# Kernel optimization log

Hardware: AMD Instinct MI355X
Metric: run time of the kernel (lower is better)

## Reference

```python
import math
import jax, jax.numpy as jnp
import numpy as np

NUM_BUCKETS = 32
MAX_DISTANCE = 128


def _relative_position_bucket(relative_position):
    # bidirectional=False: positive relative positions map to bucket 0
    rp = -jnp.minimum(relative_position, 0)  # non-negative distances
    max_exact = NUM_BUCKETS // 2
    is_small = rp < max_exact
    # clamp to >=1 before log to avoid log(0); those lanes are selected away by is_small
    rp_large = max_exact + (
        jnp.log(jnp.maximum(rp, 1).astype(jnp.float32) / max_exact)
        / math.log(MAX_DISTANCE / max_exact)
        * (NUM_BUCKETS - max_exact)
    ).astype(jnp.int32)
    rp_large = jnp.minimum(rp_large, NUM_BUCKETS - 1)
    return jnp.where(is_small, rp, rp_large)


def setup_inputs() -> dict:
    key = jax.random.key(0)
    k1, k2, k3, k4 = jax.random.split(key, 4)
    B, L, H, E = 4, 2048, 8, 64
    return {
        "queries": jax.random.normal(k1, (B, L, H, E), dtype=jnp.float32),
        "keys": jax.random.normal(k2, (B, L, H, E), dtype=jnp.float32),
        "values": jax.random.normal(k3, (B, L, H, E), dtype=jnp.float32),
        "bias_table": jax.random.normal(k4, (NUM_BUCKETS, 8), dtype=jnp.float32),
    }


def reference(queries, keys, values, bias_table):
    B, L, H, E = queries.shape
    scale = 1.0 / math.sqrt(E)

    # scores: [B, H, L, S]
    scores = jnp.einsum("blhe,bshe->bhls", queries, keys)

    # causal mask (TriangularCausalMask): masked positions -> -inf BEFORE scaling
    causal = jnp.triu(jnp.ones((L, L), dtype=bool), k=1)  # [L, L]
    scores = jnp.where(causal[None, None], -jnp.inf, scores)

    attn = scale * scores

    # T5-style relative position bias: [1, H, L, L]
    pos = jnp.arange(L)
    rel_pos = pos[None, :] - pos[:, None]  # memory - query
    buckets = _relative_position_bucket(rel_pos)  # [L, L] in [0, 32)
    bias = bias_table[buckets]  # [L, L, 8]
    bias = jnp.transpose(bias, (2, 0, 1))[None]  # [1, 8, L, L]
    attn = attn + bias

    series = jax.nn.softmax(attn, axis=-1)  # dropout p=0.0 -> identity
    V = jnp.einsum("bhls,bshd->blhd", series, values)
    return V
```

## Files before the change

kernel.cpp:

```cpp
#include <hip/hip_runtime.h>
#include <hip/hip_bf16.h>
#include <math.h>

typedef __attribute__((ext_vector_type(8)))  short short8;
typedef __attribute__((ext_vector_type(4)))  float floatx4;
typedef __attribute__((ext_vector_type(16))) float f32x16;

#define L_SEQ 2048
#define NHEADS 8
#define EDIM 64
#define PLANE (L_SEQ * EDIM)
#define LOG2E 1.4426950408889634f

union U8 { unsigned u[4]; short8 s; };

__device__ __forceinline__ unsigned cvt_pk(float lo, float hi) {
    unsigned r;
    asm("v_cvt_pk_bf16_f32 %0, %1, %2" : "=v"(r) : "v"(lo), "v"(hi));
    return r;
}
__device__ __forceinline__ short8 pack8(floatx4 a, floatx4 b) {
    U8 r;
    r.u[0] = cvt_pk(a[0], a[1]); r.u[1] = cvt_pk(a[2], a[3]);
    r.u[2] = cvt_pk(b[0], b[1]); r.u[3] = cvt_pk(b[2], b[3]);
    return r.s;
}
__device__ __forceinline__ float fast_exp2(float x) {
    float r;
    asm("v_exp_f32 %0, %1" : "=v"(r) : "v"(x));
    return r;
}

__global__ __launch_bounds__(256) void prep_frag(
    const float* __restrict__ K, const float* __restrict__ V,
    const float* __restrict__ table,
    unsigned short* __restrict__ Kf, unsigned short* __restrict__ Vf,
    float* __restrict__ Btab)
{
    __shared__ unsigned short Tk[64][72];
    __shared__ unsigned short Tv[64][72];
    const int st  = blockIdx.x;
    const int bh  = blockIdx.y;
    const int b   = bh >> 3, h = bh & 7;
    const int tid = threadIdx.x;
    const int sb  = st * 64;

    if (st == 0 && bh < 8) {
        for (int d = tid; d < L_SEQ; d += 256) {
            int bucket;
            if (d < 16) bucket = d;
            else {
                float t = logf((float)d * 0.0625f) / 2.0794415416798357f * 16.0f;
                int bb = 16 + (int)t;
                bucket = bb < 31 ? bb : 31;
            }
            Btab[bh * L_SEQ + d] = table[bucket * NHEADS + bh] * LOG2E;
        }
    }

    {
        int s0 = tid >> 3, e0 = (tid & 7) * 8;
        #pragma unroll
        for (int j = 0; j < 2; ++j) {
            int s = s0 + j * 32;
            const float* kp = K + ((size_t)(b * L_SEQ + sb + s) * NHEADS + h) * EDIM + e0;
            floatx4 f0 = *(const floatx4*)kp;
            floatx4 f1 = *(const floatx4*)(kp + 4);
            *(short8*)&Tk[s][e0] = pack8(f0, f1);
        }
    }
    {
        int e = tid & 63, sg = tid >> 6;
        #pragma unroll
        for (int j = 0; j < 16; ++j) {
            int s = sg * 16 + j;
            float v = V[((size_t)(b * L_SEQ + sb + s) * NHEADS + h) * EDIM + e];
            union { float f; unsigned u; } cv; cv.f = v;
            Tv[e][s] = (unsigned short)((cv.u + 0x7FFFu + ((cv.u >> 16) & 1u)) >> 16);
        }
    }
    __syncthreads();
    {
        int s2 = tid >> 7, t7 = tid & 127, ec = t7 >> 5, l31 = t7 & 31;
        #pragma unroll
        for (int hi = 0; hi < 2; ++hi) {
            int row = s2 * 32 + l31, e = ec * 16 + hi * 8;
            short8 v = *(const short8*)&Tk[row][e];
            size_t unit = (((size_t)bh * 64 + st * 2 + s2) * 4 + ec) * 64 + hi * 32 + l31;
            *(short8*)&Kf[unit * 8] = v;
        }
    }
    {
        int s2 = tid >> 7, t7 = tid & 127, et = t7 >> 6, lane = t7 & 63;
        #pragma unroll
        for (int c = 0; c < 2; ++c) {
            int e = et * 32 + (lane & 31), k0 = s2 * 32 + c * 16 + (lane >> 5) * 8;
            short8 v = *(const short8*)&Tv[e][k0];
            size_t unit = ((((size_t)bh * 64 + st * 2 + s2) * 2 + et) * 2 + c) * 64 + lane;
            *(short8*)&Vf[unit * 8] = v;
        }
    }
}

__global__ __launch_bounds__(256, 3) void attn_fwd(
    const float* __restrict__ Q, const unsigned short* __restrict__ Kf,
    const unsigned short* __restrict__ Vf, const float* __restrict__ Btab,
    float* __restrict__ Out)
{
    __shared__ __align__(16) float bias_lds[L_SEQ];
    __shared__ __align__(16) float osc[2][32][64];
    __shared__ float lsc[2][2][16];

    const int bid  = blockIdx.x;
    const int wid  = (bid & 7) * 128 + (bid >> 3);
    const int bh   = wid >> 5;
    const int pair = wid & 31;
    const int qgA  = pair, qgB = 63 - pair;
    const int b    = bh >> 3, h = bh & 7;
    const int tid  = threadIdx.x;
    const int w    = tid >> 6, lane = tid & 63;
    const int q32  = lane & 31;
    const int hi   = lane >> 5;
    const int hi4  = 4 * hi, hi8 = 8 * hi;

    const int dmax4 = (32 * (qgB + 1)) >> 2;
    const floatx4* bt = (const floatx4*)(Btab + h * L_SEQ);
    for (int i = tid; i < dmax4; i += 256)
        ((floatx4*)bias_lds)[i] = bt[i];
    __syncthreads();

    const float cbias = bias_lds[1024];

    const unsigned short* kfb = Kf + (size_t)bh * PLANE + lane * 8;
    const unsigned short* vfb = Vf + (size_t)bh * PLANE + lane * 8;

    U8 onesf;
    onesf.u[0] = 0x3F803F80u; onesf.u[1] = 0x3F803F80u;
    onesf.u[2] = 0x3F803F80u; onesf.u[3] = 0x3F803F80u;

    const float qscale = 0.125f * LOG2E;

    #pragma unroll 1
    for (int pass = 0; pass < 2; ++pass) {
        const int qg   = pass ? qgB : qgA;
        const int qs   = qg * 32;
        const int qrow = qs + q32;
        const int nsub = qg + 1;

        const float* qptr = Q + ((size_t)(b * L_SEQ + qrow) * NHEADS + h) * EDIM;
        short8 qfrag[4];
        #pragma unroll
        for (int ec = 0; ec < 4; ++ec) {
            floatx4 f0 = *(const floatx4*)(qptr + ec * 16 + hi8);
            floatx4 f1 = *(const floatx4*)(qptr + ec * 16 + hi8 + 4);
            qfrag[ec] = pack8(f0, f1);
        }

        const int len = (nsub + 3) >> 2;
        const int r0  = w * len;
        const int r1  = (r0 + len < nsub) ? r0 + len : nsub;

        f32x16 o_acc[2] = {};
        f32x16 o_l = {};

        for (int s32 = r0; s32 < r1; ++s32) {
            const int kv0s = s32 * 32;
            const bool far = (s32 <= qg - 5);

            const unsigned short* kp = kfb + (size_t)s32 * 2048;
            const unsigned short* vp = vfb + (size_t)s32 * 2048;
            short8 kf0 = *(const short8*)(kp);
            short8 kf1 = *(const short8*)(kp + 512);
            short8 kf2 = *(const short8*)(kp + 1024);
            short8 kf3 = *(const short8*)(kp + 1536);
            short8 vf0 = *(const short8*)(vp);
            short8 vf1 = *(const short8*)(vp + 512);
            short8 vf2 = *(const short8*)(vp + 1024);
            short8 vf3 = *(const short8*)(vp + 1536);

            f32x16 st = {};
            st = __builtin_amdgcn_mfma_f32_32x32x16_bf16(kf0, qfrag[0], st, 0, 0, 0);
            st = __builtin_amdgcn_mfma_f32_32x32x16_bf16(kf1, qfrag[1], st, 0, 0, 0);
            st = __builtin_amdgcn_mfma_f32_32x32x16_bf16(kf2, qfrag[2], st, 0, 0, 0);
            st = __builtin_amdgcn_mfma_f32_32x32x16_bf16(kf3, qfrag[3], st, 0, 0, 0);

            float p[16];
            if (far) {
                #pragma unroll
                for (int r = 0; r < 16; ++r)
                    p[r] = fast_exp2(fmaf(qscale, st[r], cbias));
            } else if (s32 != qg) {
                const float* bptr = &bias_lds[qrow - kv0s - hi4];
                #pragma unroll
                for (int r = 0; r < 16; ++r)
                    p[r] = fast_exp2(fmaf(qscale, st[r], bptr[-(r & 3) - 8 * (r >> 2)]));
            } else {
                #pragma unroll
                for (int r = 0; r < 16; ++r) {
                    int kidx = (r & 3) + 8 * (r >> 2) + hi4;
                    int d = q32 - kidx;
                    int dc = d < 0 ? 0 : d;
                    float ex = fast_exp2(fmaf(qscale, st[r], bias_lds[dc]));
                    p[r] = (d >= 0) ? ex : 0.0f;
                }
            }

            unsigned x0 = cvt_pk(p[0],  p[1]),  x1 = cvt_pk(p[2],  p[3]);
            unsigned y0 = cvt_pk(p[4],  p[5]),  y1 = cvt_pk(p[6],  p[7]);
            unsigned x2 = cvt_pk(p[8],  p[9]),  x3 = cvt_pk(p[10], p[11]);
            unsigned y2 = cvt_pk(p[12], p[13]), y3 = cvt_pk(p[14], p[15]);
            asm("v_permlane32_swap_b32 %0, %1" : "+v"(x0), "+v"(y0));
            asm("v_permlane32_swap_b32 %0, %1" : "+v"(x1), "+v"(y1));
            asm("v_permlane32_swap_b32 %0, %1" : "+v"(x2), "+v"(y2));
            asm("v_permlane32_swap_b32 %0, %1" : "+v"(x3), "+v"(y3));
            U8 pf0;
            pf0.u[0] = x0; pf0.u[1] = x1; pf0.u[2] = y0; pf0.u[3] = y1;
            U8 pf1;
            pf1.u[0] = x2; pf1.u[1] = x3; pf1.u[2] = y2; pf1.u[3] = y3;

            o_acc[0] = __builtin_amdgcn_mfma_f32_32x32x16_bf16(pf0.s, vf0, o_acc[0], 0, 0, 0);
            o_acc[0] = __builtin_amdgcn_mfma_f32_32x32x16_bf16(pf1.s, vf1, o_acc[0], 0, 0, 0);
            o_acc[1] = __builtin_amdgcn_mfma_f32_32x32x16_bf16(pf0.s, vf2, o_acc[1], 0, 0, 0);
            o_acc[1] = __builtin_amdgcn_mfma_f32_32x32x16_bf16(pf1.s, vf3, o_acc[1], 0, 0, 0);
            o_l      = __builtin_amdgcn_mfma_f32_32x32x16_bf16(pf0.s, onesf.s, o_l, 0, 0, 0);
            o_l      = __builtin_amdgcn_mfma_f32_32x32x16_bf16(pf1.s, onesf.s, o_l, 0, 0, 0);
        }

        __syncthreads();
        if (w & 1) {
            int slot = w >> 1;
            #pragma unroll
            for (int et = 0; et < 2; ++et)
                #pragma unroll
                for (int r = 0; r < 16; ++r)
                    osc[slot][et * 16 + r][lane] = o_acc[et][r];
            if (q32 == 0) {
                #pragma unroll
                for (int r = 0; r < 16; ++r) lsc[slot][hi][r] = o_l[r];
            }
        }
        __syncthreads();
        if (!(w & 1)) {
            int slot = w >> 1;
            #pragma unroll
            for (int et = 0; et < 2; ++et)
                #pragma unroll
                for (int r = 0; r < 16; ++r)
                    o_acc[et][r] += osc[slot][et * 16 + r][lane];
            #pragma unroll
            for (int r = 0; r < 16; ++r) o_l[r] += lsc[slot][hi][r];
        }
        __syncthreads();
        if (w == 2) {
            #pragma unroll
            for (int et = 0; et < 2; ++et)
                #pragma unroll
                for (int r = 0; r < 16; ++r)
                    osc[0][et * 16 + r][lane] = o_acc[et][r];
            if (q32 == 0) {
                #pragma unroll
                for (int r = 0; r < 16; ++r) lsc[0][hi][r] = o_l[r];
            }
        }
        __syncthreads();
        if (w == 0) {
            #pragma unroll
            for (int et = 0; et < 2; ++et)
                #pragma unroll
                for (int r = 0; r < 16; ++r)
                    o_acc[et][r] += osc[0][et * 16 + r][lane];
            #pragma unroll
            for (int r = 0; r < 16; ++r) o_l[r] += lsc[0][hi][r];

            #pragma unroll
            for (int r = 0; r < 16; ++r) {
                int qv = (r & 3) + 8 * (r >> 2) + hi4;
                float iv = 1.0f / o_l[r];
                float* op = Out + ((size_t)(b * L_SEQ + qs + qv) * NHEADS + h) * EDIM + q32;
                op[0]  = o_acc[0][r] * iv;
                op[32] = o_acc[1][r] * iv;
            }
        }
    }
}

extern "C" void kernel_launch(void* const* d_in, const int* in_sizes, int n_in,
                              void* d_out, int out_size, void* d_ws, size_t ws_size,
                              hipStream_t stream) {
    const float* Q     = (const float*)d_in[0];
    const float* K     = (const float*)d_in[1];
    const float* V     = (const float*)d_in[2];
    const float* table = (const float*)d_in[3];
    float* Out = (float*)d_out;
    unsigned short* Kf = (unsigned short*)d_ws;
    unsigned short* Vf = Kf + (size_t)4 * NHEADS * PLANE;
    float* Btab = (float*)(Vf + (size_t)4 * NHEADS * PLANE);
    (void)in_sizes; (void)n_in; (void)out_size; (void)ws_size;

    dim3 pgrid(32, 32);
    prep_frag<<<pgrid, 256, 0, stream>>>(K, V, table, Kf, Vf, Btab);
    attn_fwd<<<dim3(1024), 256, 0, stream>>>(Q, Kf, Vf, Btab, Out);
}
```

Measured before the change: 57.82 us.

## Process two adjacent query tiles per pass to reuse K/V fragment loads

```diff
diff --git a/kernel.cpp b/kernel.cpp
--- a/kernel.cpp
+++ b/kernel.cpp
@@ -102,7 +102,7 @@
     }
 }
 
-__global__ __launch_bounds__(256, 3) void attn_fwd(
+__global__ __launch_bounds__(256, 2) void attn_fwd(
     const float* __restrict__ Q, const unsigned short* __restrict__ Kf,
     const unsigned short* __restrict__ Vf, const float* __restrict__ Btab,
     float* __restrict__ Out)
@@ -112,10 +112,9 @@
     __shared__ float lsc[2][2][16];
 
     const int bid  = blockIdx.x;
-    const int wid  = (bid & 7) * 128 + (bid >> 3);
-    const int bh   = wid >> 5;
-    const int pair = wid & 31;
-    const int qgA  = pair, qgB = 63 - pair;
+    const int wid  = (bid & 7) * 64 + (bid >> 3);
+    const int bh   = wid >> 4;
+    const int pj   = wid & 15;
     const int b    = bh >> 3, h = bh & 7;
     const int tid  = threadIdx.x;
     const int w    = tid >> 6, lane = tid & 63;
@@ -123,7 +122,9 @@
     const int hi   = lane >> 5;
     const int hi4  = 4 * hi, hi8 = 8 * hi;
 
-    const int dmax4 = (32 * (qgB + 1)) >> 2;
+    const int n0 = 2 * pj + 2, n1 = 64 - 2 * pj;
+    const int nmax = n0 > n1 ? n0 : n1;
+    const int dmax4 = (32 * nmax) >> 2;
     const floatx4* bt = (const floatx4*)(Btab + h * L_SEQ);
     for (int i = tid; i < dmax4; i += 256)
         ((floatx4*)bias_lds)[i] = bt[i];
@@ -140,147 +141,169 @@
 
     const float qscale = 0.125f * LOG2E;
 
+    short8 vf0, vf1, vf2, vf3;
+
+    auto sm_pv = [&](const f32x16& st, int qrowX, int qgX, int s32,
+                     f32x16* o_acc, f32x16& o_l) {
+        const int kv0s = s32 * 32;
+        float p[16];
+        if (s32 <= qgX - 5) {
+            #pragma unroll
+            for (int r = 0; r < 16; ++r)
+                p[r] = fast_exp2(fmaf(qscale, st[r], cbias));
+        } else if (s32 != qgX) {
+            const float* bptr = &bias_lds[qrowX - kv0s - hi4];
+            #pragma unroll
+            for (int r = 0; r < 16; ++r)
+                p[r] = fast_exp2(fmaf(qscale, st[r], bptr[-(r & 3) - 8 * (r >> 2)]));
+        } else {
+            #pragma unroll
+            for (int r = 0; r < 16; ++r) {
+                int kidx = (r & 3) + 8 * (r >> 2) + hi4;
+                int d = q32 - kidx;
+                int dc = d < 0 ? 0 : d;
+                float ex = fast_exp2(fmaf(qscale, st[r], bias_lds[dc]));
+                p[r] = (d >= 0) ? ex : 0.0f;
+            }
+        }
+        unsigned x0 = cvt_pk(p[0],  p[1]),  x1 = cvt_pk(p[2],  p[3]);
+        unsigned y0 = cvt_pk(p[4],  p[5]),  y1 = cvt_pk(p[6],  p[7]);
+        unsigned x2 = cvt_pk(p[8],  p[9]),  x3 = cvt_pk(p[10], p[11]);
+        unsigned y2 = cvt_pk(p[12], p[13]), y3 = cvt_pk(p[14], p[15]);
+        asm("v_permlane32_swap_b32 %0, %1" : "+v"(x0), "+v"(y0));
+        asm("v_permlane32_swap_b32 %0, %1" : "+v"(x1), "+v"(y1));
+        asm("v_permlane32_swap_b32 %0, %1" : "+v"(x2), "+v"(y2));
+        asm("v_permlane32_swap_b32 %0, %1" : "+v"(x3), "+v"(y3));
+        U8 pf0; pf0.u[0] = x0; pf0.u[1] = x1; pf0.u[2] = y0; pf0.u[3] = y1;
+        U8 pf1; pf1.u[0] = x2; pf1.u[1] = x3; pf1.u[2] = y2; pf1.u[3] = y3;
+
+        o_acc[0] = __builtin_amdgcn_mfma_f32_32x32x16_bf16(pf0.s, vf0, o_acc[0], 0, 0, 0);
+        o_acc[0] = __builtin_amdgcn_mfma_f32_32x32x16_bf16(pf1.s, vf1, o_acc[0], 0, 0, 0);
+        o_acc[1] = __builtin_amdgcn_mfma_f32_32x32x16_bf16(pf0.s, vf2, o_acc[1], 0, 0, 0);
+        o_acc[1] = __builtin_amdgcn_mfma_f32_32x32x16_bf16(pf1.s, vf3, o_acc[1], 0, 0, 0);
+        o_l      = __builtin_amdgcn_mfma_f32_32x32x16_bf16(pf0.s, onesf.s, o_l, 0, 0, 0);
+        o_l      = __builtin_amdgcn_mfma_f32_32x32x16_bf16(pf1.s, onesf.s, o_l, 0, 0, 0);
+    };
+
+    auto merge_store = [&](f32x16* o_acc, f32x16& o_l, int qsX) {
+        __syncthreads();
+        if (w & 1) {
+            int slot = w >> 1;
+            #pragma unroll
+            for (int et = 0; et < 2; ++et)
+                #pragma unroll
+                for (int r = 0; r < 16; ++r)
+                    osc[slot][et * 16 + r][lane] = o_acc[et][r];
+            if (q32 == 0) {
+                #pragma unroll
+                for (int r = 0; r < 16; ++r) lsc[slot][hi][r] = o_l[r];
+            }
+        }
+        __syncthreads();
+        if (!(w & 1)) {
+            int slot = w >> 1;
+            #pragma unroll
+            for (int et = 0; et < 2; ++et)
+                #pragma unroll
+                for (int r = 0; r < 16; ++r)
+                    o_acc[et][r] += osc[slot][et * 16 + r][lane];
+            #pragma unroll
+            for (int r = 0; r < 16; ++r) o_l[r] += lsc[slot][hi][r];
+        }
+        __syncthreads();
+        if (w == 2) {
+            #pragma unroll
+            for (int et = 0; et < 2; ++et)
+                #pragma unroll
+                for (int r = 0; r < 16; ++r)
+                    osc[0][et * 16 + r][lane] = o_acc[et][r];
+            if (q32 == 0) {
+                #pragma unroll
+                for (int r = 0; r < 16; ++r) lsc[0][hi][r] = o_l[r];
+            }
+        }
+        __syncthreads();
+        if (w == 0) {
+            #pragma unroll
+            for (int et = 0; et < 2; ++et)
+                #pragma unroll
+                for (int r = 0; r < 16; ++r)
+                    o_acc[et][r] += osc[0][et * 16 + r][lane];
+            #pragma unroll
+            for (int r = 0; r < 16; ++r) o_l[r] += lsc[0][hi][r];
+
+            #pragma unroll
+            for (int r = 0; r < 16; ++r) {
+                int qv = (r & 3) + 8 * (r >> 2) + hi4;
+                float iv = 1.0f / o_l[r];
+                float* op = Out + ((size_t)(b * L_SEQ + qsX + qv) * NHEADS + h) * EDIM + q32;
+                op[0]  = o_acc[0][r] * iv;
+                op[32] = o_acc[1][r] * iv;
+            }
+        }
+    };
+
     #pragma unroll 1
     for (int pass = 0; pass < 2; ++pass) {
-        const int qg   = pass ? qgB : qgA;
-        const int qs   = qg * 32;
-        const int qrow = qs + q32;
-        const int nsub = qg + 1;
-
-        const float* qptr = Q + ((size_t)(b * L_SEQ + qrow) * NHEADS + h) * EDIM;
-        short8 qfrag[4];
+        const int g0   = pass ? (62 - 2 * pj) : (2 * pj);
+        const int qgA  = g0, qgB = g0 + 1;
+        const int qsA  = qgA * 32, qsB = qgB * 32;
+        const int qrowA = qsA + q32, qrowB = qsB + q32;
+        const int nsub = qgB + 1;
+
+        const float* qpA = Q + ((size_t)(b * L_SEQ + qrowA) * NHEADS + h) * EDIM;
+        const float* qpB = Q + ((size_t)(b * L_SEQ + qrowB) * NHEADS + h) * EDIM;
+        short8 qfragA[4], qfragB[4];
         #pragma unroll
         for (int ec = 0; ec < 4; ++ec) {
-            floatx4 f0 = *(const floatx4*)(qptr + ec * 16 + hi8);
-            floatx4 f1 = *(const floatx4*)(qptr + ec * 16 + hi8 + 4);
-            qfrag[ec] = pack8(f0, f1);
+            floatx4 a0 = *(const floatx4*)(qpA + ec * 16 + hi8);
+            floatx4 a1 = *(const floatx4*)(qpA + ec * 16 + hi8 + 4);
+            qfragA[ec] = pack8(a0, a1);
+            floatx4 b0 = *(const floatx4*)(qpB + ec * 16 + hi8);
+            floatx4 b1 = *(const floatx4*)(qpB + ec * 16 + hi8 + 4);
+            qfragB[ec] = pack8(b0, b1);
         }
 
         const int len = (nsub + 3) >> 2;
         const int r0  = w * len;
         const int r1  = (r0 + len < nsub) ? r0 + len : nsub;
 
-        f32x16 o_acc[2] = {};
-        f32x16 o_l = {};
+        f32x16 oA[2] = {}, oB[2] = {};
+        f32x16 olA = {}, olB = {};
 
         for (int s32 = r0; s32 < r1; ++s32) {
-            const int kv0s = s32 * 32;
-            const bool far = (s32 <= qg - 5);
-
             const unsigned short* kp = kfb + (size_t)s32 * 2048;
             const unsigned short* vp = vfb + (size_t)s32 * 2048;
             short8 kf0 = *(const short8*)(kp);
             short8 kf1 = *(const short8*)(kp + 512);
             short8 kf2 = *(const short8*)(kp + 1024);
             short8 kf3 = *(const short8*)(kp + 1536);
-            short8 vf0 = *(const short8*)(vp);
-            short8 vf1 = *(const short8*)(vp + 512);
-            short8 vf2 = *(const short8*)(vp + 1024);
-            short8 vf3 = *(const short8*)(vp + 1536);
-
-            f32x16 st = {};
-            st = __builtin_amdgcn_mfma_f32_32x32x16_bf16(kf0, qfrag[0], st, 0, 0, 0);
-            st = __builtin_amdgcn_mfma_f32_32x32x16_bf16(kf1, qfrag[1], st, 0, 0, 0);
-            st = __builtin_amdgcn_mfma_f32_32x32x16_bf16(kf2, qfrag[2], st, 0, 0, 0);
-            st = __builtin_amdgcn_mfma_f32_32x32x16_bf16(kf3, qfrag[3], st, 0, 0, 0);
-
-            float p[16];
-            if (far) {
-                #pragma unroll
-                for (int r = 0; r < 16; ++r)
-                    p[r] = fast_exp2(fmaf(qscale, st[r], cbias));
-            } else if (s32 != qg) {
-                const float* bptr = &bias_lds[qrow - kv0s - hi4];
-                #pragma unroll
-                for (int r = 0; r < 16; ++r)
-                    p[r] = fast_exp2(fmaf(qscale, st[r], bptr[-(r & 3) - 8 * (r >> 2)]));
-            } else {
-                #pragma unroll
-                for (int r = 0; r < 16; ++r) {
-                    int kidx = (r & 3) + 8 * (r >> 2) + hi4;
-                    int d = q32 - kidx;
-                    int dc = d < 0 ? 0 : d;
-                    float ex = fast_exp2(fmaf(qscale, st[r], bias_lds[dc]));
-                    p[r] = (d >= 0) ? ex : 0.0f;
-                }
-            }
-
-            unsigned x0 = cvt_pk(p[0],  p[1]),  x1 = cvt_pk(p[2],  p[3]);
-            unsigned y0 = cvt_pk(p[4],  p[5]),  y1 = cvt_pk(p[6],  p[7]);
-            unsigned x2 = cvt_pk(p[8],  p[9]),  x3 = cvt_pk(p[10], p[11]);
-            unsigned y2 = cvt_pk(p[12], p[13]), y3 = cvt_pk(p[14], p[15]);
-            asm("v_permlane32_swap_b32 %0, %1" : "+v"(x0), "+v"(y0));
-            asm("v_permlane32_swap_b32 %0, %1" : "+v"(x1), "+v"(y1));
-            asm("v_permlane32_swap_b32 %0, %1" : "+v"(x2), "+v"(y2));
-            asm("v_permlane32_swap_b32 %0, %1" : "+v"(x3), "+v"(y3));
-            U8 pf0;
-            pf0.u[0] = x0; pf0.u[1] = x1; pf0.u[2] = y0; pf0.u[3] = y1;
-            U8 pf1;
-            pf1.u[0] = x2; pf1.u[1] = x3; pf1.u[2] = y2; pf1.u[3] = y3;
-
-            o_acc[0] = __builtin_amdgcn_mfma_f32_32x32x16_bf16(pf0.s, vf0, o_acc[0], 0, 0, 0);
-            o_acc[0] = __builtin_amdgcn_mfma_f32_32x32x16_bf16(pf1.s, vf1, o_acc[0], 0, 0, 0);
-            o_acc[1] = __builtin_amdgcn_mfma_f32_32x32x16_bf16(pf0.s, vf2, o_acc[1], 0, 0, 0);
-            o_acc[1] = __builtin_amdgcn_mfma_f32_32x32x16_bf16(pf1.s, vf3, o_acc[1], 0, 0, 0);
-            o_l      = __builtin_amdgcn_mfma_f32_32x32x16_bf16(pf0.s, onesf.s, o_l, 0, 0, 0);
-            o_l      = __builtin_amdgcn_mfma_f32_32x32x16_bf16(pf1.s, onesf.s, o_l, 0, 0, 0);
-        }
-
-        __syncthreads();
-        if (w & 1) {
-            int slot = w >> 1;
-            #pragma unroll
-            for (int et = 0; et < 2; ++et)
-                #pragma unroll
-                for (int r = 0; r < 16; ++r)
-                    osc[slot][et * 16 + r][lane] = o_acc[et][r];
-            if (q32 == 0) {
-                #pragma unroll
-                for (int r = 0; r < 16; ++r) lsc[slot][hi][r] = o_l[r];
-            }
-        }
-        __syncthreads();
-        if (!(w & 1)) {
-            int slot = w >> 1;
-            #pragma unroll
-            for (int et = 0; et < 2; ++et)
-                #pragma unroll
-                for (int r = 0; r < 16; ++r)
-                    o_acc[et][r] += osc[slot][et * 16 + r][lane];
-            #pragma unroll
-            for (int r = 0; r < 16; ++r) o_l[r] += lsc[slot][hi][r];
-        }
-        __syncthreads();
-        if (w == 2) {
-            #pragma unroll
-            for (int et = 0; et < 2; ++et)
-                #pragma unroll
-                for (int r = 0; r < 16; ++r)
-                    osc[0][et * 16 + r][lane] = o_acc[et][r];
-            if (q32 == 0) {
-                #pragma unroll
-                for (int r = 0; r < 16; ++r) lsc[0][hi][r] = o_l[r];
-            }
-        }
-        __syncthreads();
-        if (w == 0) {
-            #pragma unroll
-            for (int et = 0; et < 2; ++et)
-                #pragma unroll
-                for (int r = 0; r < 16; ++r)
-                    o_acc[et][r] += osc[0][et * 16 + r][lane];
-            #pragma unroll
-            for (int r = 0; r < 16; ++r) o_l[r] += lsc[0][hi][r];
-
-            #pragma unroll
-            for (int r = 0; r < 16; ++r) {
-                int qv = (r & 3) + 8 * (r >> 2) + hi4;
-                float iv = 1.0f / o_l[r];
-                float* op = Out + ((size_t)(b * L_SEQ + qs + qv) * NHEADS + h) * EDIM + q32;
-                op[0]  = o_acc[0][r] * iv;
-                op[32] = o_acc[1][r] * iv;
-            }
-        }
+            vf0 = *(const short8*)(vp);
+            vf1 = *(const short8*)(vp + 512);
+            vf2 = *(const short8*)(vp + 1024);
+            vf3 = *(const short8*)(vp + 1536);
+
+            const bool doA = (s32 <= qgA);
+
+            f32x16 stB = {};
+            stB = __builtin_amdgcn_mfma_f32_32x32x16_bf16(kf0, qfragB[0], stB, 0, 0, 0);
+            stB = __builtin_amdgcn_mfma_f32_32x32x16_bf16(kf1, qfragB[1], stB, 0, 0, 0);
+            stB = __builtin_amdgcn_mfma_f32_32x32x16_bf16(kf2, qfragB[2], stB, 0, 0, 0);
+            stB = __builtin_amdgcn_mfma_f32_32x32x16_bf16(kf3, qfragB[3], stB, 0, 0, 0);
+            f32x16 stA = {};
+            if (doA) {
+                stA = __builtin_amdgcn_mfma_f32_32x32x16_bf16(kf0, qfragA[0], stA, 0, 0, 0);
+                stA = __builtin_amdgcn_mfma_f32_32x32x16_bf16(kf1, qfragA[1], stA, 0, 0, 0);
+                stA = __builtin_amdgcn_mfma_f32_32x32x16_bf16(kf2, qfragA[2], stA, 0, 0, 0);
+                stA = __builtin_amdgcn_mfma_f32_32x32x16_bf16(kf3, qfragA[3], stA, 0, 0, 0);
+            }
+
+            sm_pv(stB, qrowB, qgB, s32, oB, olB);
+            if (doA) sm_pv(stA, qrowA, qgA, s32, oA, olA);
+        }
+
+        merge_store(oA, olA, qsA);
+        merge_store(oB, olB, qsB);
     }
 }
 
@@ -299,5 +322,5 @@
 
     dim3 pgrid(32, 32);
     prep_frag<<<pgrid, 256, 0, stream>>>(K, V, table, Kf, Vf, Btab);
-    attn_fwd<<<dim3(1024), 256, 0, stream>>>(Q, Kf, Vf, Btab, Out);
-}
+    attn_fwd<<<dim3(512), 256, 0, stream>>>(Q, Kf, Vf, Btab, Out);
+}
```

New measurement: 53.15 us. 8.1% less time.
